# Kernel optimization log

Hardware: AMD Instinct MI355X
Metric: run time of the kernel (lower is better)

## Reference

```python
import jax, jax.numpy as jnp
import numpy as np

N, E = 50000, 800000
IN_DIM, HID_DIM, OUT_DIM = 512, 256, 128


def setup_inputs() -> dict:
    key = jax.random.key(0)
    ks = jax.random.split(key, 10)
    x = jax.random.normal(ks[0], (N, IN_DIM), dtype=jnp.float32)
    edge_index = jax.random.randint(ks[1], (2, E), 0, N, dtype=jnp.int64)
    edge_weight = jax.random.uniform(ks[2], (E,), dtype=jnp.float32)
    # GCNConv weights (PyG stores weight as [in, out]; out = x @ W + b)
    def glorot(k, fan_in, fan_out):
        lim = np.sqrt(6.0 / (fan_in + fan_out)).astype(np.float32)
        return jax.random.uniform(k, (fan_in, fan_out), minval=-lim, maxval=lim, dtype=jnp.float32)
    W1 = glorot(ks[3], IN_DIM, HID_DIM)
    b1 = jnp.zeros((HID_DIM,), dtype=jnp.float32)
    W2 = glorot(ks[4], HID_DIM, OUT_DIM)
    b2 = jnp.zeros((OUT_DIM,), dtype=jnp.float32)
    Wp = glorot(ks[5], OUT_DIM, OUT_DIM)
    bp = jnp.zeros((OUT_DIM,), dtype=jnp.float32)
    return {"x": x, "edge_index": edge_index, "edge_weight": edge_weight,
            "W1": W1, "b1": b1, "W2": W2, "b2": b2, "Wp": Wp, "bp": bp}


def _gcn_norm(edge_index, edge_weight, n_nodes):
    # add self loops with weight 1.0 (PyG gcn_norm, fill_value=1.0)
    loops = jnp.arange(n_nodes, dtype=edge_index.dtype)
    row = jnp.concatenate([edge_index[0], loops])
    col = jnp.concatenate([edge_index[1], loops])
    w = jnp.concatenate([edge_weight, jnp.ones((n_nodes,), edge_weight.dtype)])
    deg = jax.ops.segment_sum(w, col, num_segments=n_nodes)  # [N]
    dinv = jnp.where(deg > 0, jax.lax.rsqrt(deg), 0.0)
    norm = dinv[row] * w * dinv[col]  # [E+N]
    return row, col, norm


def _gcn_conv(h, row, col, norm, W, b, n_nodes):
    h = h @ W                              # [N, out]
    msgs = h[row] * norm[:, None]          # gather + scale  [E+N, out]
    out = jax.ops.segment_sum(msgs, col, num_segments=n_nodes)  # scatter-add
    return out + b


def reference(x, edge_index, edge_weight, W1, b1, W2, b2, Wp, bp):
    n_nodes = x.shape[0]
    # eval mode: F.dropout(edge_weight, training=False) is identity
    row, col, norm = _gcn_norm(edge_index, edge_weight, n_nodes)
    h = jax.nn.relu(_gcn_conv(x, row, col, norm, W1, b1, n_nodes))
    # eval mode: F.dropout identity
    h = _gcn_conv(h, row, col, norm, W2, b2, n_nodes)
    return h @ Wp + bp
```

## Files before the change

### kernel.cpp

```cpp
#include <hip/hip_runtime.h>

#define IN_DIM 512
#define HID_DIM 256
#define OUT_DIM 128
#define BCAP 64

typedef unsigned short u16;
typedef __attribute__((ext_vector_type(8))) short bf16x8;
typedef __attribute__((ext_vector_type(4))) float f32x4;

__device__ inline u16 f2bf(float f) {
    unsigned u = __float_as_uint(f);
    return (u16)((u + 0x7FFFu + ((u >> 16) & 1u)) >> 16);
}
__device__ inline float bf2f(u16 u) {
    return __uint_as_float(((unsigned)u) << 16);
}

__device__ inline void gld_lds16(const void* g, void* l) {
    __builtin_amdgcn_global_load_lds((const __attribute__((address_space(1))) unsigned*)g,
                                     (__attribute__((address_space(3))) unsigned*)l, 16, 0, 0);
}


__global__ void bucket_fill_kernel(const int* __restrict__ row, const int* __restrict__ col,
                                   const float* __restrict__ w,
                                   int* __restrict__ cnt, int2* __restrict__ bucket, int E) {
    int e = blockIdx.x * blockDim.x + threadIdx.x;
    if (e >= E) return;
    int c = col[e];
    int slot = atomicAdd(&cnt[c], 1);
    if (slot < BCAP) {
        int2 v;
        v.x = row[e];
        v.y = __float_as_int(w[e]);
        bucket[(size_t)c * BCAP + slot] = v;
    }
}

__global__ void deg_dinv_kernel(const int2* __restrict__ bucket, const int* __restrict__ cnt,
                                float* __restrict__ dinv, int n) {
    int i = blockIdx.x * blockDim.x + threadIdx.x;
    if (i >= n) return;
    int c = min(cnt[i], BCAP);
    const int2* b = bucket + (size_t)i * BCAP;
    float s = 1.0f;
    for (int p = 0; p < c; ++p) s += __int_as_float(b[p].y);
    dinv[i] = (s > 0.0f) ? rsqrtf(s) : 0.0f;
}


__global__ void convert_x_kernel(const float* __restrict__ X, u16* __restrict__ Xb,
                                 int M, int Mpad) {
    long tid = (long)blockIdx.x * blockDim.x + threadIdx.x;
    long total = (long)Mpad * IN_DIM / 8;
    if (tid >= total) return;
    long base = tid * 8;
    int r = (int)(base / IN_DIM);
    ushort4 lo, hi;
    if (r < M) {
        float4 f0 = *(const float4*)(X + base);
        float4 f1 = *(const float4*)(X + base + 4);
        lo.x = f2bf(f0.x); lo.y = f2bf(f0.y); lo.z = f2bf(f0.z); lo.w = f2bf(f0.w);
        hi.x = f2bf(f1.x); hi.y = f2bf(f1.y); hi.z = f2bf(f1.z); hi.w = f2bf(f1.w);
    } else {
        lo.x = lo.y = lo.z = lo.w = 0;
        hi.x = hi.y = hi.z = hi.w = 0;
    }
    *(ushort4*)(Xb + base) = lo;
    *(ushort4*)(Xb + base + 4) = hi;
}

__global__ void transpose_bf_kernel(const float* __restrict__ W, u16* __restrict__ WT,
                                    int K, int Nc) {
    int idx = blockIdx.x * blockDim.x + threadIdx.x;
    if (idx >= K * Nc) return;
    int nrow = idx / K, k = idx - nrow * K;
    WT[idx] = f2bf(W[(size_t)k * Nc + nrow]);
}


#define TM 128
#define TN 128
#define TK 32

template <typename OutT>
__global__ __launch_bounds__(256)
void mfma_gemm_kernel(const u16* __restrict__ A, const u16* __restrict__ BT,
                      const float* __restrict__ bias, OutT* __restrict__ C,
                      int M, int Nc, int K) {
    __shared__ u16 As[TM * TK];
    __shared__ u16 Bs[TN * TK];
    const int tid = threadIdx.x;
    const int w = tid >> 6, l = tid & 63;
    const int wr = w >> 1, wc = w & 1;
    const long tile_m = (long)blockIdx.x * TM;
    const int tile_n = blockIdx.y * TN;

    const int r0 = w * 32 + (l >> 2);
    const int r1 = r0 + 16;
    const int c0 = l & 3;
    const long ga0 = (tile_m + r0) * (long)K + (long)((c0 ^ (r0 & 3)) * 8);
    const long ga1 = (tile_m + r1) * (long)K + (long)((c0 ^ (r1 & 3)) * 8);
    const long gb0 = (long)(tile_n + r0) * K + (long)((c0 ^ (r0 & 3)) * 8);
    const long gb1 = (long)(tile_n + r1) * K + (long)((c0 ^ (r1 & 3)) * 8);
    u16* ldsA0 = &As[(w * 2 + 0) * 512];
    u16* ldsA1 = &As[(w * 2 + 1) * 512];
    u16* ldsB0 = &Bs[(w * 2 + 0) * 512];
    u16* ldsB1 = &Bs[(w * 2 + 1) * 512];

    f32x4 acc[4][4] = {};
    const int lr = l & 15;
    const int kl = l >> 4;

    for (int k0 = 0; k0 < K; k0 += TK) {
        if (k0) __syncthreads();
        gld_lds16(A + ga0 + k0, ldsA0);
        gld_lds16(A + ga1 + k0, ldsA1);
        gld_lds16(BT + gb0 + k0, ldsB0);
        gld_lds16(BT + gb1 + k0, ldsB1);
        __syncthreads();

        bf16x8 af[4], bfv[4];
#pragma unroll
        for (int mi = 0; mi < 4; ++mi) {
            int rowi = wr * 64 + mi * 16 + lr;
            int byte = rowi * 64 + ((kl ^ (rowi & 3)) * 16);
            af[mi] = *(const bf16x8*)((const char*)As + byte);
        }
#pragma unroll
        for (int ni = 0; ni < 4; ++ni) {
            int rowi = wc * 64 + ni * 16 + lr;
            int byte = rowi * 64 + ((kl ^ (rowi & 3)) * 16);
            bfv[ni] = *(const bf16x8*)((const char*)Bs + byte);
        }
#pragma unroll
        for (int mi = 0; mi < 4; ++mi)
#pragma unroll
            for (int ni = 0; ni < 4; ++ni)
                acc[mi][ni] = __builtin_amdgcn_mfma_f32_16x16x32_bf16(af[mi], bfv[ni], acc[mi][ni], 0, 0, 0);
    }

    float bv[4];
#pragma unroll
    for (int ni = 0; ni < 4; ++ni)
        bv[ni] = bias ? bias[tile_n + wc * 64 + ni * 16 + lr] : 0.0f;
#pragma unroll
    for (int mi = 0; mi < 4; ++mi) {
#pragma unroll
        for (int reg = 0; reg < 4; ++reg) {
            long rowg = tile_m + wr * 64 + mi * 16 + kl * 4 + reg;
            if (rowg < M) {
#pragma unroll
                for (int ni = 0; ni < 4; ++ni) {
                    int colc = tile_n + wc * 64 + ni * 16 + lr;
                    float v = acc[mi][ni][reg] + bv[ni];
                    if constexpr (sizeof(OutT) == 2) C[rowg * Nc + colc] = f2bf(v);
                    else                             C[rowg * Nc + colc] = v;
                }
            }
        }
    }
}


template <int DIM, bool RELU>
__global__ __launch_bounds__(256)
void aggregate_kernel(const u16* __restrict__ t,
                      const int2* __restrict__ bucket,
                      const int* __restrict__ cnt,
                      const float* __restrict__ dinv,
                      const float* __restrict__ bias,
                      u16* __restrict__ out_bf, int n) {
    constexpr int V = DIM / 64;
    const int wv = threadIdx.x >> 6;
    const int l = threadIdx.x & 63;
    const int node = blockIdx.x * 4 + wv;
    if (node >= n) return;
    const float dv = dinv[node];
    const float dv2 = dv * dv;
    float acc[V];
    if constexpr (V == 4) {
        ushort4 q = *(const ushort4*)(t + (size_t)node * DIM + l * 4);
        acc[0] = dv2 * bf2f(q.x); acc[1] = dv2 * bf2f(q.y);
        acc[2] = dv2 * bf2f(q.z); acc[3] = dv2 * bf2f(q.w);
    } else {
        ushort2 q = *(const ushort2*)(t + (size_t)node * DIM + l * 2);
        acc[0] = dv2 * bf2f(q.x); acc[1] = dv2 * bf2f(q.y);
    }
    const int e = min(cnt[node], BCAP);
    const int2* b = bucket + (size_t)node * BCAP;
    int p = 0;
    for (; p + 4 <= e; p += 4) {
        int2 e0 = b[p], e1 = b[p + 1], e2 = b[p + 2], e3 = b[p + 3];
        float w0 = dv * __int_as_float(e0.y) * dinv[e0.x];
        float w1 = dv * __int_as_float(e1.y) * dinv[e1.x];
        float w2 = dv * __int_as_float(e2.y) * dinv[e2.x];
        float w3 = dv * __int_as_float(e3.y) * dinv[e3.x];
        if constexpr (V == 4) {
            ushort4 q0 = *(const ushort4*)(t + (size_t)e0.x * DIM + l * 4);
            ushort4 q1 = *(const ushort4*)(t + (size_t)e1.x * DIM + l * 4);
            ushort4 q2 = *(const ushort4*)(t + (size_t)e2.x * DIM + l * 4);
            ushort4 q3 = *(const ushort4*)(t + (size_t)e3.x * DIM + l * 4);
            acc[0] = fmaf(w0, bf2f(q0.x), acc[0]); acc[1] = fmaf(w0, bf2f(q0.y), acc[1]);
            acc[2] = fmaf(w0, bf2f(q0.z), acc[2]); acc[3] = fmaf(w0, bf2f(q0.w), acc[3]);
            acc[0] = fmaf(w1, bf2f(q1.x), acc[0]); acc[1] = fmaf(w1, bf2f(q1.y), acc[1]);
            acc[2] = fmaf(w1, bf2f(q1.z), acc[2]); acc[3] = fmaf(w1, bf2f(q1.w), acc[3]);
            acc[0] = fmaf(w2, bf2f(q2.x), acc[0]); acc[1] = fmaf(w2, bf2f(q2.y), acc[1]);
            acc[2] = fmaf(w2, bf2f(q2.z), acc[2]); acc[3] = fmaf(w2, bf2f(q2.w), acc[3]);
            acc[0] = fmaf(w3, bf2f(q3.x), acc[0]); acc[1] = fmaf(w3, bf2f(q3.y), acc[1]);
            acc[2] = fmaf(w3, bf2f(q3.z), acc[2]); acc[3] = fmaf(w3, bf2f(q3.w), acc[3]);
        } else {
            ushort2 q0 = *(const ushort2*)(t + (size_t)e0.x * DIM + l * 2);
            ushort2 q1 = *(const ushort2*)(t + (size_t)e1.x * DIM + l * 2);
            ushort2 q2 = *(const ushort2*)(t + (size_t)e2.x * DIM + l * 2);
            ushort2 q3 = *(const ushort2*)(t + (size_t)e3.x * DIM + l * 2);
            acc[0] = fmaf(w0, bf2f(q0.x), acc[0]); acc[1] = fmaf(w0, bf2f(q0.y), acc[1]);
            acc[0] = fmaf(w1, bf2f(q1.x), acc[0]); acc[1] = fmaf(w1, bf2f(q1.y), acc[1]);
            acc[0] = fmaf(w2, bf2f(q2.x), acc[0]); acc[1] = fmaf(w2, bf2f(q2.y), acc[1]);
            acc[0] = fmaf(w3, bf2f(q3.x), acc[0]); acc[1] = fmaf(w3, bf2f(q3.y), acc[1]);
        }
    }
    for (; p < e; ++p) {
        int2 e0 = b[p];
        float wgt = dv * __int_as_float(e0.y) * dinv[e0.x];
        if constexpr (V == 4) {
            ushort4 q = *(const ushort4*)(t + (size_t)e0.x * DIM + l * 4);
            acc[0] = fmaf(wgt, bf2f(q.x), acc[0]); acc[1] = fmaf(wgt, bf2f(q.y), acc[1]);
            acc[2] = fmaf(wgt, bf2f(q.z), acc[2]); acc[3] = fmaf(wgt, bf2f(q.w), acc[3]);
        } else {
            ushort2 q = *(const ushort2*)(t + (size_t)e0.x * DIM + l * 2);
            acc[0] = fmaf(wgt, bf2f(q.x), acc[0]); acc[1] = fmaf(wgt, bf2f(q.y), acc[1]);
        }
    }
#pragma unroll
    for (int j = 0; j < V; ++j) {
        float v = acc[j] + bias[l * V + j];
        if (RELU) v = fmaxf(v, 0.0f);
        acc[j] = v;
    }
    if constexpr (V == 4) {
        ushort4 st;
        st.x = f2bf(acc[0]); st.y = f2bf(acc[1]); st.z = f2bf(acc[2]); st.w = f2bf(acc[3]);
        *(ushort4*)(out_bf + (size_t)node * DIM + l * 4) = st;
    } else {
        ushort2 st;
        st.x = f2bf(acc[0]); st.y = f2bf(acc[1]);
        *(ushort2*)(out_bf + (size_t)node * DIM + l * 2) = st;
    }
}


extern "C" void kernel_launch(void* const* d_in, const int* in_sizes, int n_in,
                              void* d_out, int out_size, void* d_ws, size_t ws_size,
                              hipStream_t stream) {
    const float* x  = (const float*)d_in[0];
    const int*   ei = (const int*)d_in[1];
    const float* ew = (const float*)d_in[2];
    const float* W1 = (const float*)d_in[3];
    const float* b1 = (const float*)d_in[4];
    const float* W2 = (const float*)d_in[5];
    const float* b2 = (const float*)d_in[6];
    const float* Wp = (const float*)d_in[7];
    const float* bp = (const float*)d_in[8];
    float* out = (float*)d_out;

    const int E = in_sizes[2];
    const int N = in_sizes[0] / IN_DIM;
    const int Mpad = ((N + TM - 1) / TM) * TM;
    const int* row = ei;
    const int* col = ei + E;

    size_t off = 0;
    auto carve = [&](size_t bytes) -> void* {
        void* p = (char*)d_ws + off;
        off += (bytes + 255) & ~(size_t)255;
        return p;
    };
    float* dinv   = (float*)carve((size_t)N * 4);
    int*   cnt    = (int*)carve((size_t)N * 4);
    int2*  bucket = (int2*)carve((size_t)N * BCAP * 8);
    u16*   W1T    = (u16*)carve((size_t)HID_DIM * IN_DIM * 2);
    u16*   W2T    = (u16*)carve((size_t)OUT_DIM * HID_DIM * 2);
    u16*   WpT    = (u16*)carve((size_t)OUT_DIM * OUT_DIM * 2);
    u16*   bufA   = (u16*)carve((size_t)Mpad * IN_DIM * 2);
    u16*   bufB   = (u16*)carve((size_t)Mpad * HID_DIM * 2);

    u16* x_bf = bufA;
    u16* t1   = bufB;
    u16* a1   = bufA;
    u16* t2   = bufB;
    u16* a2   = bufA;

    const int TB = 256;
    const int gN = (N + TB - 1) / TB;
    const int gE = (E + TB - 1) / TB;

    hipMemsetAsync(cnt, 0, (size_t)N * 4, stream);
    bucket_fill_kernel<<<gE, TB, 0, stream>>>(row, col, ew, cnt, bucket, E);
    deg_dinv_kernel<<<gN, TB, 0, stream>>>(bucket, cnt, dinv, N);

    convert_x_kernel<<<(int)(((long)Mpad * IN_DIM / 8 + TB - 1) / TB), TB, 0, stream>>>(x, x_bf, N, Mpad);
    transpose_bf_kernel<<<(IN_DIM * HID_DIM + TB - 1) / TB, TB, 0, stream>>>(W1, W1T, IN_DIM, HID_DIM);
    transpose_bf_kernel<<<(HID_DIM * OUT_DIM + TB - 1) / TB, TB, 0, stream>>>(W2, W2T, HID_DIM, OUT_DIM);
    transpose_bf_kernel<<<(OUT_DIM * OUT_DIM + TB - 1) / TB, TB, 0, stream>>>(Wp, WpT, OUT_DIM, OUT_DIM);

    const int gm = Mpad / TM;
    const int gagg = (N + 3) / 4;

    mfma_gemm_kernel<u16><<<dim3(gm, HID_DIM / TN), 256, 0, stream>>>(x_bf, W1T, nullptr, t1, Mpad, HID_DIM, IN_DIM);
    aggregate_kernel<HID_DIM, true><<<gagg, 256, 0, stream>>>(t1, bucket, cnt, dinv, b1, a1, N);
    mfma_gemm_kernel<u16><<<dim3(gm, OUT_DIM / TN), 256, 0, stream>>>(a1, W2T, nullptr, t2, Mpad, OUT_DIM, HID_DIM);
    aggregate_kernel<OUT_DIM, false><<<gagg, 256, 0, stream>>>(t2, bucket, cnt, dinv, b2, a2, N);
    mfma_gemm_kernel<float><<<dim3(gm, OUT_DIM / TN), 256, 0, stream>>>(a2, WpT, bp, out, N, OUT_DIM, OUT_DIM);
}
```

Measured before the change: 394.4 us.

## Fold projection weight into second GCN layer and unroll aggregation by eight

```diff
diff --git a/kernel.cpp b/kernel.cpp
--- a/kernel.cpp
+++ b/kernel.cpp
@@ -79,6 +79,27 @@
     WT[idx] = f2bf(W[(size_t)k * Nc + nrow]);
 }
 
+__global__ void fuse_w2p_kernel(const float* __restrict__ W2, const float* __restrict__ Wp,
+                                u16* __restrict__ W2pT) {
+    int idx = blockIdx.x * blockDim.x + threadIdx.x;
+    if (idx >= OUT_DIM * HID_DIM) return;
+    int n = idx / HID_DIM, k = idx - n * HID_DIM;
+    float s = 0.0f;
+    for (int m = 0; m < OUT_DIM; ++m)
+        s = fmaf(W2[(size_t)k * OUT_DIM + m], Wp[(size_t)m * OUT_DIM + n], s);
+    W2pT[idx] = f2bf(s);
+}
+
+__global__ void fuse_bias2_kernel(const float* __restrict__ b2, const float* __restrict__ Wp,
+                                  const float* __restrict__ bp, float* __restrict__ bias2) {
+    int n = blockIdx.x * blockDim.x + threadIdx.x;
+    if (n >= OUT_DIM) return;
+    float s = bp[n];
+    for (int m = 0; m < OUT_DIM; ++m)
+        s = fmaf(b2[m], Wp[(size_t)m * OUT_DIM + n], s);
+    bias2[n] = s;
+}
+
 
 #define TM 128
 #define TN 128
@@ -164,14 +185,14 @@
 }
 
 
-template <int DIM, bool RELU>
+template <int DIM, bool RELU, typename OutT>
 __global__ __launch_bounds__(256)
 void aggregate_kernel(const u16* __restrict__ t,
                       const int2* __restrict__ bucket,
                       const int* __restrict__ cnt,
                       const float* __restrict__ dinv,
                       const float* __restrict__ bias,
-                      u16* __restrict__ out_bf, int n) {
+                      OutT* __restrict__ outp, int n) {
     constexpr int V = DIM / 64;
     const int wv = threadIdx.x >> 6;
     const int l = threadIdx.x & 63;
@@ -191,34 +212,62 @@
     const int e = min(cnt[node], BCAP);
     const int2* b = bucket + (size_t)node * BCAP;
     int p = 0;
+    for (; p + 8 <= e; p += 8) {
+        int2 ed[8];
+        float wt[8];
+#pragma unroll
+        for (int j = 0; j < 8; ++j) ed[j] = b[p + j];
+#pragma unroll
+        for (int j = 0; j < 8; ++j) wt[j] = dv * __int_as_float(ed[j].y) * dinv[ed[j].x];
+        if constexpr (V == 4) {
+            ushort4 q[8];
+#pragma unroll
+            for (int j = 0; j < 8; ++j) q[j] = *(const ushort4*)(t + (size_t)ed[j].x * DIM + l * 4);
+#pragma unroll
+            for (int j = 0; j < 8; ++j) {
+                acc[0] = fmaf(wt[j], bf2f(q[j].x), acc[0]);
+                acc[1] = fmaf(wt[j], bf2f(q[j].y), acc[1]);
+                acc[2] = fmaf(wt[j], bf2f(q[j].z), acc[2]);
+                acc[3] = fmaf(wt[j], bf2f(q[j].w), acc[3]);
+            }
+        } else {
+            ushort2 q[8];
+#pragma unroll
+            for (int j = 0; j < 8; ++j) q[j] = *(const ushort2*)(t + (size_t)ed[j].x * DIM + l * 2);
+#pragma unroll
+            for (int j = 0; j < 8; ++j) {
+                acc[0] = fmaf(wt[j], bf2f(q[j].x), acc[0]);
+                acc[1] = fmaf(wt[j], bf2f(q[j].y), acc[1]);
+            }
+        }
+    }
     for (; p + 4 <= e; p += 4) {
-        int2 e0 = b[p], e1 = b[p + 1], e2 = b[p + 2], e3 = b[p + 3];
-        float w0 = dv * __int_as_float(e0.y) * dinv[e0.x];
-        float w1 = dv * __int_as_float(e1.y) * dinv[e1.x];
-        float w2 = dv * __int_as_float(e2.y) * dinv[e2.x];
-        float w3 = dv * __int_as_float(e3.y) * dinv[e3.x];
-        if constexpr (V == 4) {
-            ushort4 q0 = *(const ushort4*)(t + (size_t)e0.x * DIM + l * 4);
-            ushort4 q1 = *(const ushort4*)(t + (size_t)e1.x * DIM + l * 4);
-            ushort4 q2 = *(const ushort4*)(t + (size_t)e2.x * DIM + l * 4);
-            ushort4 q3 = *(const ushort4*)(t + (size_t)e3.x * DIM + l * 4);
-            acc[0] = fmaf(w0, bf2f(q0.x), acc[0]); acc[1] = fmaf(w0, bf2f(q0.y), acc[1]);
-            acc[2] = fmaf(w0, bf2f(q0.z), acc[2]); acc[3] = fmaf(w0, bf2f(q0.w), acc[3]);
-            acc[0] = fmaf(w1, bf2f(q1.x), acc[0]); acc[1] = fmaf(w1, bf2f(q1.y), acc[1]);
-            acc[2] = fmaf(w1, bf2f(q1.z), acc[2]); acc[3] = fmaf(w1, bf2f(q1.w), acc[3]);
-            acc[0] = fmaf(w2, bf2f(q2.x), acc[0]); acc[1] = fmaf(w2, bf2f(q2.y), acc[1]);
-            acc[2] = fmaf(w2, bf2f(q2.z), acc[2]); acc[3] = fmaf(w2, bf2f(q2.w), acc[3]);
-            acc[0] = fmaf(w3, bf2f(q3.x), acc[0]); acc[1] = fmaf(w3, bf2f(q3.y), acc[1]);
-            acc[2] = fmaf(w3, bf2f(q3.z), acc[2]); acc[3] = fmaf(w3, bf2f(q3.w), acc[3]);
-        } else {
-            ushort2 q0 = *(const ushort2*)(t + (size_t)e0.x * DIM + l * 2);
-            ushort2 q1 = *(const ushort2*)(t + (size_t)e1.x * DIM + l * 2);
-            ushort2 q2 = *(const ushort2*)(t + (size_t)e2.x * DIM + l * 2);
-            ushort2 q3 = *(const ushort2*)(t + (size_t)e3.x * DIM + l * 2);
-            acc[0] = fmaf(w0, bf2f(q0.x), acc[0]); acc[1] = fmaf(w0, bf2f(q0.y), acc[1]);
-            acc[0] = fmaf(w1, bf2f(q1.x), acc[0]); acc[1] = fmaf(w1, bf2f(q1.y), acc[1]);
-            acc[0] = fmaf(w2, bf2f(q2.x), acc[0]); acc[1] = fmaf(w2, bf2f(q2.y), acc[1]);
-            acc[0] = fmaf(w3, bf2f(q3.x), acc[0]); acc[1] = fmaf(w3, bf2f(q3.y), acc[1]);
+        int2 ed[4];
+        float wt[4];
+#pragma unroll
+        for (int j = 0; j < 4; ++j) ed[j] = b[p + j];
+#pragma unroll
+        for (int j = 0; j < 4; ++j) wt[j] = dv * __int_as_float(ed[j].y) * dinv[ed[j].x];
+        if constexpr (V == 4) {
+            ushort4 q[4];
+#pragma unroll
+            for (int j = 0; j < 4; ++j) q[j] = *(const ushort4*)(t + (size_t)ed[j].x * DIM + l * 4);
+#pragma unroll
+            for (int j = 0; j < 4; ++j) {
+                acc[0] = fmaf(wt[j], bf2f(q[j].x), acc[0]);
+                acc[1] = fmaf(wt[j], bf2f(q[j].y), acc[1]);
+                acc[2] = fmaf(wt[j], bf2f(q[j].z), acc[2]);
+                acc[3] = fmaf(wt[j], bf2f(q[j].w), acc[3]);
+            }
+        } else {
+            ushort2 q[4];
+#pragma unroll
+            for (int j = 0; j < 4; ++j) q[j] = *(const ushort2*)(t + (size_t)ed[j].x * DIM + l * 2);
+#pragma unroll
+            for (int j = 0; j < 4; ++j) {
+                acc[0] = fmaf(wt[j], bf2f(q[j].x), acc[0]);
+                acc[1] = fmaf(wt[j], bf2f(q[j].y), acc[1]);
+            }
         }
     }
     for (; p < e; ++p) {
@@ -239,14 +288,24 @@
         if (RELU) v = fmaxf(v, 0.0f);
         acc[j] = v;
     }
-    if constexpr (V == 4) {
-        ushort4 st;
-        st.x = f2bf(acc[0]); st.y = f2bf(acc[1]); st.z = f2bf(acc[2]); st.w = f2bf(acc[3]);
-        *(ushort4*)(out_bf + (size_t)node * DIM + l * 4) = st;
+    if constexpr (sizeof(OutT) == 2) {
+        if constexpr (V == 4) {
+            ushort4 st;
+            st.x = f2bf(acc[0]); st.y = f2bf(acc[1]); st.z = f2bf(acc[2]); st.w = f2bf(acc[3]);
+            *(ushort4*)((u16*)outp + (size_t)node * DIM + l * 4) = st;
+        } else {
+            ushort2 st;
+            st.x = f2bf(acc[0]); st.y = f2bf(acc[1]);
+            *(ushort2*)((u16*)outp + (size_t)node * DIM + l * 2) = st;
+        }
     } else {
-        ushort2 st;
-        st.x = f2bf(acc[0]); st.y = f2bf(acc[1]);
-        *(ushort2*)(out_bf + (size_t)node * DIM + l * 2) = st;
+        if constexpr (V == 4) {
+            float4 st = {acc[0], acc[1], acc[2], acc[3]};
+            *(float4*)((float*)outp + (size_t)node * DIM + l * 4) = st;
+        } else {
+            float2 st = {acc[0], acc[1]};
+            *(float2*)((float*)outp + (size_t)node * DIM + l * 2) = st;
+        }
     }
 }
 
@@ -281,16 +340,15 @@
     int*   cnt    = (int*)carve((size_t)N * 4);
     int2*  bucket = (int2*)carve((size_t)N * BCAP * 8);
     u16*   W1T    = (u16*)carve((size_t)HID_DIM * IN_DIM * 2);
-    u16*   W2T    = (u16*)carve((size_t)OUT_DIM * HID_DIM * 2);
-    u16*   WpT    = (u16*)carve((size_t)OUT_DIM * OUT_DIM * 2);
+    u16*   W2pT   = (u16*)carve((size_t)OUT_DIM * HID_DIM * 2);
+    float* bias2  = (float*)carve((size_t)OUT_DIM * 4);
     u16*   bufA   = (u16*)carve((size_t)Mpad * IN_DIM * 2);
     u16*   bufB   = (u16*)carve((size_t)Mpad * HID_DIM * 2);
 
     u16* x_bf = bufA;
     u16* t1   = bufB;
     u16* a1   = bufA;
-    u16* t2   = bufB;
-    u16* a2   = bufA;
+    u16* t3   = bufB;
 
     const int TB = 256;
     const int gN = (N + TB - 1) / TB;
@@ -302,15 +360,14 @@
 
     convert_x_kernel<<<(int)(((long)Mpad * IN_DIM / 8 + TB - 1) / TB), TB, 0, stream>>>(x, x_bf, N, Mpad);
     transpose_bf_kernel<<<(IN_DIM * HID_DIM + TB - 1) / TB, TB, 0, stream>>>(W1, W1T, IN_DIM, HID_DIM);
-    transpose_bf_kernel<<<(HID_DIM * OUT_DIM + TB - 1) / TB, TB, 0, stream>>>(W2, W2T, HID_DIM, OUT_DIM);
-    transpose_bf_kernel<<<(OUT_DIM * OUT_DIM + TB - 1) / TB, TB, 0, stream>>>(Wp, WpT, OUT_DIM, OUT_DIM);
+    fuse_w2p_kernel<<<(OUT_DIM * HID_DIM + TB - 1) / TB, TB, 0, stream>>>(W2, Wp, W2pT);
+    fuse_bias2_kernel<<<1, OUT_DIM, 0, stream>>>(b2, Wp, bp, bias2);
 
     const int gm = Mpad / TM;
     const int gagg = (N + 3) / 4;
 
     mfma_gemm_kernel<u16><<<dim3(gm, HID_DIM / TN), 256, 0, stream>>>(x_bf, W1T, nullptr, t1, Mpad, HID_DIM, IN_DIM);
-    aggregate_kernel<HID_DIM, true><<<gagg, 256, 0, stream>>>(t1, bucket, cnt, dinv, b1, a1, N);
-    mfma_gemm_kernel<u16><<<dim3(gm, OUT_DIM / TN), 256, 0, stream>>>(a1, W2T, nullptr, t2, Mpad, OUT_DIM, HID_DIM);
-    aggregate_kernel<OUT_DIM, false><<<gagg, 256, 0, stream>>>(t2, bucket, cnt, dinv, b2, a2, N);
-    mfma_gemm_kernel<float><<<dim3(gm, OUT_DIM / TN), 256, 0, stream>>>(a2, WpT, bp, out, N, OUT_DIM, OUT_DIM);
-}
+    aggregate_kernel<HID_DIM, true, u16><<<gagg, 256, 0, stream>>>(t1, bucket, cnt, dinv, b1, a1, N);
+    mfma_gemm_kernel<u16><<<dim3(gm, OUT_DIM / TN), 256, 0, stream>>>(a1, W2pT, nullptr, t3, Mpad, OUT_DIM, HID_DIM);
+    aggregate_kernel<OUT_DIM, false, float><<<gagg, 256, 0, stream>>>(t3, bucket, cnt, dinv, bias2, out, N);
+}
```

Measured after the change: 391.0 us. About the same (-0.8%).
